# Optimization experiments

Hardware: AMD Instinct MI355X
Metric: run time of the kernel (lower is better)

The kernel has to match this reference:

```python
import jax, jax.numpy as jnp
import numpy as np

N_NODES = 50000
N_EDGES = 800000
NODE_DIM = 128
EDGE_DIM = 16
OUT_DIM = 64
HEADS = 4


def setup_inputs() -> dict:
    key = jax.random.key(0)
    ks = jax.random.split(key, 12)
    x = jax.random.normal(ks[0], (N_NODES, NODE_DIM), jnp.float32)
    edge_index = jax.random.randint(ks[1], (2, N_EDGES), 0, N_NODES)
    batch = jnp.zeros((N_NODES,), jnp.int32)
    edge_attr = jax.random.normal(ks[2], (N_EDGES, EDGE_DIM), jnp.float32)
    s = 1.0 / np.sqrt(NODE_DIM)
    W = jax.random.normal(ks[3], (NODE_DIM, HEADS * OUT_DIM), jnp.float32) * s
    att_src = jax.random.normal(ks[4], (HEADS, OUT_DIM), jnp.float32) * 0.1
    att_dst = jax.random.normal(ks[5], (HEADS, OUT_DIM), jnp.float32) * 0.1
    W_e = jax.random.normal(ks[6], (EDGE_DIM, HEADS * OUT_DIM), jnp.float32) * (1.0 / np.sqrt(EDGE_DIM))
    att_edge = jax.random.normal(ks[7], (HEADS, OUT_DIM), jnp.float32) * 0.1
    bias = jnp.zeros((OUT_DIM,), jnp.float32)
    gamma = jnp.ones((OUT_DIM,), jnp.float32)
    beta = jnp.zeros((OUT_DIM,), jnp.float32)
    return {"x": x, "edge_index": edge_index, "batch": batch, "edge_attr": edge_attr,
            "W": W, "att_src": att_src, "att_dst": att_dst, "W_e": W_e,
            "att_edge": att_edge, "bias": bias, "gamma": gamma, "beta": beta}


def reference(x, edge_index, batch, edge_attr, W, att_src, att_dst, W_e, att_edge, bias, gamma, beta):
    N = x.shape[0]
    H, C = att_src.shape
    src, dst = edge_index[0], edge_index[1]
    E = src.shape[0]

    # add self loops; self-loop edge_attr = per-node mean of incoming edge attrs (PyG fill_value='mean')
    cnt = jax.ops.segment_sum(jnp.ones((E, 1), x.dtype), dst, num_segments=N)
    loop_attr = jax.ops.segment_sum(edge_attr, dst, num_segments=N) / jnp.maximum(cnt, 1.0)
    loop_idx = jnp.arange(N, dtype=src.dtype)
    src_f = jnp.concatenate([src, loop_idx])
    dst_f = jnp.concatenate([dst, loop_idx])
    ea = jnp.concatenate([edge_attr, loop_attr], axis=0)

    h = (x @ W).reshape(N, H, C)                       # [N,H,C]
    a_src = jnp.einsum('nhc,hc->nh', h, att_src)       # [N,H]
    a_dst = jnp.einsum('nhc,hc->nh', h, att_dst)
    e_emb = (ea @ W_e).reshape(-1, H, C)               # [E',H,C]
    a_edge = jnp.einsum('ehc,hc->eh', e_emb, att_edge)

    alpha = jax.nn.leaky_relu(a_src[src_f] + a_dst[dst_f] + a_edge, 0.2)  # [E',H]
    amax = jax.ops.segment_max(alpha, dst_f, num_segments=N)
    expa = jnp.exp(alpha - amax[dst_f])
    denom = jax.ops.segment_sum(expa, dst_f, num_segments=N)
    att = expa / (denom[dst_f] + 1e-16)                # segment softmax over dst

    msg = h[src_f] * att[:, :, None]                   # [E',H,C]
    out = jax.ops.segment_sum(msg, dst_f, num_segments=N)  # [N,H,C]
    out = out.mean(axis=1) + bias                      # concat=False -> head mean

    mu = out.mean(-1, keepdims=True)
    var = out.var(-1, keepdims=True)
    out = (out - mu) / jnp.sqrt(var + 1e-5) * gamma + beta
    return jax.nn.elu(out)
```

## Files before the change

kernel.cpp:

```cpp
#include <hip/hip_runtime.h>

typedef unsigned int u32;
typedef unsigned short u16;

static constexpr int NN  = 50000;
static constexpr int EE  = 800000;
static constexpr int CAP = 64;

typedef __attribute__((ext_vector_type(8))) short bf16x8;
typedef __attribute__((ext_vector_type(4))) float f32x4;
typedef __attribute__((ext_vector_type(4))) u32   u32x4;

__device__ inline float u2f(u32 u){ union{u32 i; float f;} v; v.i=u; return v.f; }
__device__ inline float bf2f(u16 u){ return u2f(((u32)u)<<16); }
__device__ inline u16 f2bf(float f){ union{float f; u32 i;} v; v.f=f; u32 i=v.i;
    return (u16)((i + 0x7fffu + ((i>>16)&1u))>>16); }
__device__ inline u32 pk2(float a, float b){ return (u32)f2bf(a) | ((u32)f2bf(b)<<16); }
__device__ inline float lrelu(float x){ return x > 0.f ? x : 0.2f*x; }

__device__ inline u32 pkh(float a, float b){
    union{ _Float16 h[2]; u32 u; } v;
    v.h[0] = (_Float16)a; v.h[1] = (_Float16)b;
    return v.u;
}
__device__ inline float hlo(u32 u){ union{u32 u; _Float16 h[2];} v; v.u=u; return (float)v.h[0]; }
__device__ inline float hhi(u32 u){ union{u32 u; _Float16 h[2];} v; v.u=u; return (float)v.h[1]; }

__device__ inline float ld(const void* base, size_t i, int f32m){
    return f32m ? ((const float*)base)[i] : bf2f(((const u16*)base)[i]);
}

__device__ inline float wsum(float v){
    #pragma unroll
    for (int m=1;m<64;m<<=1) v += __shfl_xor(v, m, 64);
    return v;
}

#if defined(__has_builtin)
#if __has_builtin(__builtin_amdgcn_fdot2_f32_bf16)
#define HAS_DOT2 1
#endif
#endif

#ifdef HAS_DOT2
typedef __attribute__((ext_vector_type(2))) __bf16 bf16x2;
#endif

__device__ inline float dot2acc(u32 hv, u32 wv, float acc){
#ifdef HAS_DOT2
    union { u32 u; bf16x2 v; } a, b; a.u = hv; b.u = wv;
    return __builtin_amdgcn_fdot2_f32_bf16(a.v, b.v, acc, false);
#else
    acc = fmaf(u2f(hv<<16),         u2f(wv<<16),         acc);
    acc = fmaf(u2f(hv&0xffff0000u), u2f(wv&0xffff0000u), acc);
    return acc;
#endif
}

__device__ inline int detect_f32(const u16* xraw){
    int lane = threadIdx.x & 63;
    bool bad = false;
    #pragma unroll
    for (int i = 0; i < 8; ++i){
        float v = bf2f(xraw[2*(lane + i*64)]);
        if (!(fabsf(v) < 1e10f)) bad = true;
    }
    return __any(bad) ? 1 : 0;
}

__device__ inline void edge_logits(const void* ea, int e, int f32m,
                                   const float* __restrict__ Ml, float* A){
    float v[16];
    if (f32m){
        const f32x4* r = ((const f32x4*)ea) + (size_t)e*4;
        f32x4 a = __builtin_nontemporal_load(r);
        f32x4 b = __builtin_nontemporal_load(r+1);
        f32x4 c = __builtin_nontemporal_load(r+2);
        f32x4 d = __builtin_nontemporal_load(r+3);
        v[0]=a[0]; v[1]=a[1]; v[2]=a[2]; v[3]=a[3];
        v[4]=b[0]; v[5]=b[1]; v[6]=b[2]; v[7]=b[3];
        v[8]=c[0]; v[9]=c[1]; v[10]=c[2]; v[11]=c[3];
        v[12]=d[0]; v[13]=d[1]; v[14]=d[2]; v[15]=d[3];
    } else {
        const u32x4* r = ((const u32x4*)ea) + (size_t)e*2;
        u32x4 q0 = __builtin_nontemporal_load(r);
        u32x4 q1 = __builtin_nontemporal_load(r+1);
        v[0]=u2f(q0[0]<<16); v[1]=u2f(q0[0]&0xffff0000u);
        v[2]=u2f(q0[1]<<16); v[3]=u2f(q0[1]&0xffff0000u);
        v[4]=u2f(q0[2]<<16); v[5]=u2f(q0[2]&0xffff0000u);
        v[6]=u2f(q0[3]<<16); v[7]=u2f(q0[3]&0xffff0000u);
        v[8]=u2f(q1[0]<<16); v[9]=u2f(q1[0]&0xffff0000u);
        v[10]=u2f(q1[1]<<16); v[11]=u2f(q1[1]&0xffff0000u);
        v[12]=u2f(q1[2]<<16); v[13]=u2f(q1[2]&0xffff0000u);
        v[14]=u2f(q1[3]<<16); v[15]=u2f(q1[3]&0xffff0000u);
    }
    float a0=0,a1=0,a2=0,a3=0;
    #pragma unroll
    for (int j = 0; j < 16; ++j){
        a0 = fmaf(v[j], Ml[j*4+0], a0);
        a1 = fmaf(v[j], Ml[j*4+1], a1);
        a2 = fmaf(v[j], Ml[j*4+2], a2);
        a3 = fmaf(v[j], Ml[j*4+3], a3);
    }
    A[0]=a0; A[1]=a1; A[2]=a2; A[3]=a3;
}

__global__ __launch_bounds__(256) void k_prep(const u16* __restrict__ xraw,
                                              const void* __restrict__ W,
                                              const void* __restrict__ att_src,
                                              const void* __restrict__ att_dst,
                                              const void* __restrict__ W_e,
                                              const void* __restrict__ att_edge,
                                              int* __restrict__ flag,
                                              u16* __restrict__ Wt,
                                              float* __restrict__ Mv,
                                              int* __restrict__ deg){
    int f32m = detect_f32(xraw);
    int b = blockIdx.x, t = threadIdx.x;
    if (b == 0){
        if (t == 0) *flag = f32m;
        if (t < 64){
            int d = t >> 2, h = t & 3;
            float s = 0.f;
            for (int c = 0; c < 64; ++c)
                s += ld(W_e, d*256 + h*64 + c, f32m) * ld(att_edge, h*64 + c, f32m);
            Mv[t] = s;
        }
    } else if (b <= 128){
        int i = (b-1)*256 + t;
        int k = i >> 8, j = i & 255;
        int n = (j & 3)*64 + (j >> 2);
        Wt[j*128 + k] = f2bf(ld(W, (size_t)k*256 + n, f32m));
    } else if (b <= 136){
        int i = (b-129)*256 + t;
        int c = i >> 7, k = i & 127;
        float s = 0.f;
        if (c < 8){
            int h = c & 3;
            const void* att = (c < 4) ? att_src : att_dst;
            for (int j = 0; j < 64; ++j)
                s += ld(W, (size_t)k*256 + h*64 + j, f32m) * ld(att, h*64 + j, f32m);
        }
        Wt[(size_t)(256 + c)*128 + k] = f2bf(s);
    } else {
        int i = (b-137)*256 + t;
        if (i < NN) deg[i] = 0;
    }
}

__global__ __launch_bounds__(256) void k_gx(const void* __restrict__ x,
                                            const u16* __restrict__ Wt,
                                            const int* __restrict__ flag,
                                            u16* __restrict__ hbuf,
                                            float* __restrict__ a_src,
                                            float* __restrict__ a_dst,
                                            const int* __restrict__ ei,
                                            const void* __restrict__ ea,
                                            const float* __restrict__ Mv,
                                            int* __restrict__ deg,
                                            u32x4* __restrict__ erec,
                                            u32* __restrict__ bidx,
                                            int N, int E, int GB){
    int t = threadIdx.x;
    int f32m = *flag;
    int b = (int)blockIdx.x;
    bool isg; int wid;
    if (b < 2*GB){ isg = !(b & 1); wid = b >> 1; }
    else         { isg = false;    wid = b - GB; }
    if (isg){
        int row0 = wid*64;
        int wave = t >> 6, lane = t & 63;
        int l15 = lane & 15, quad = lane >> 4;
        int grow = row0 + wave*16 + l15; if (grow >= N) grow = N-1;
        bf16x8 afr[4];
        if (f32m){
            const f32x4* xf = (const f32x4*)x;
            #pragma unroll
            for (int s=0;s<4;++s){
                f32x4 v0 = __builtin_nontemporal_load(&xf[(size_t)grow*32 + s*8 + quad*2]);
                f32x4 v1 = __builtin_nontemporal_load(&xf[(size_t)grow*32 + s*8 + quad*2 + 1]);
                union{ u32x4 u; bf16x8 b; } cv;
                cv.u[0] = pk2(v0[0],v0[1]); cv.u[1] = pk2(v0[2],v0[3]);
                cv.u[2] = pk2(v1[0],v1[1]); cv.u[3] = pk2(v1[2],v1[3]);
                afr[s] = cv.b;
            }
        } else {
            const u16* x16 = (const u16*)x;
            #pragma unroll
            for (int s=0;s<4;++s)
                afr[s] = __builtin_nontemporal_load(
                    (const bf16x8*)&x16[(size_t)grow*128 + s*32 + quad*8]);
        }
        f32x4 acc[17];
        #pragma unroll
        for (int tl=0;tl<17;++tl){
            f32x4 a = {0.f,0.f,0.f,0.f};
            #pragma unroll
            for (int s=0;s<4;++s){
                bf16x8 bfr = *(const bf16x8*)&Wt[(size_t)(tl*16 + l15)*128 + s*32 + quad*8];
                a = __builtin_amdgcn_mfma_f32_16x16x32_bf16(afr[s], bfr, a, 0, 0, 0);
            }
            acc[tl] = a;
        }
        int rbase = row0 + wave*16 + quad*4;
        #pragma unroll
        for (int r=0;r<4;++r){
            int gr = rbase + r;
            if (gr < N){
                if (l15 < 4)
                    __builtin_nontemporal_store(acc[16][r], &a_src[gr*4 + l15]);
                else if (l15 < 8)
                    __builtin_nontemporal_store(acc[16][r], &a_dst[gr*4 + (l15-4)]);
            }
        }
        #pragma unroll
        for (int r=0;r<4;++r){
            int gr = rbase + r;
            if (gr < N){
                #pragma unroll
                for (int tl=0;tl<16;++tl)
                    __builtin_nontemporal_store(f2bf(acc[tl][r]),
                        &hbuf[(size_t)gr*256 + tl*16 + l15]);
            }
        }
    } else {
        int base = wid*512 + t;
        #pragma unroll
        for (int j=0;j<2;++j){
            int e = base + j*256;
            if (e >= E) continue;
            int src = __builtin_nontemporal_load(&ei[e]);
            int dst = __builtin_nontemporal_load(&ei[E + e]);
            int slot = atomicAdd(&deg[dst], 1);
            float A[4];
            edge_logits(ea, e, f32m, Mv, A);
            u32x4 rec;
            rec[0] = (u32)src; rec[1] = pkh(A[0],A[1]);
            rec[2] = pkh(A[2],A[3]); rec[3] = 0u;
            __builtin_nontemporal_store(rec, &erec[e]);
            if (slot < CAP)
                bidx[(size_t)dst*CAP + slot] = (u32)e;
        }
    }
}

__global__ __launch_bounds__(256) void k_node(const int* __restrict__ deg,
                                              const u32* __restrict__ bidx,
                                              const u32x4* __restrict__ erec,
                                              const float* __restrict__ a_src,
                                              const float* __restrict__ a_dst,
                                              const u16* __restrict__ hbuf,
                                              const void* __restrict__ bias,
                                              const void* __restrict__ gamma,
                                              const void* __restrict__ beta,
                                              const int* __restrict__ flag,
                                              void* __restrict__ out, int N){
    __shared__ uint4 lrec[4][CAP+4];
    int f32m = *flag;
    int lane = threadIdx.x & 63;
    int slot = threadIdx.x >> 6;
    int n = blockIdx.x*4 + slot;
    int dg = deg[n];
    int dc = dg < CAP ? dg : CAP;
    float4 an  = ((const float4*)a_src)[n];
    float4 adn = ((const float4*)a_dst)[n];
    bool v0 = lane < dc;
    u32 src = (u32)n;
    float w0=0.f,w1=0.f,w2=0.f,w3=0.f;
    float a0=0.f,a1=0.f,a2=0.f,a3=0.f;
    if (v0){
        u32 e = __builtin_nontemporal_load(&bidx[(size_t)n*CAP + lane]);
        u32x4 r = __builtin_nontemporal_load(&erec[e]);
        src = r[0];
        a0 = hlo(r[1]); a1 = hhi(r[1]); a2 = hlo(r[2]); a3 = hhi(r[2]);
        float4 asg = ((const float4*)a_src)[src];
        w0 = expf(lrelu(asg.x + adn.x + a0));
        w1 = expf(lrelu(asg.y + adn.y + a1));
        w2 = expf(lrelu(asg.z + adn.z + a2));
        w3 = expf(lrelu(asg.w + adn.w + a3));
    }
    float dn0 = wsum(w0), dn1 = wsum(w1), dn2 = wsum(w2), dn3 = wsum(w3);
    float invd = 1.f / (float)(dg > 1 ? dg : 1);
    float ge0 = wsum(a0)*invd, ge1 = wsum(a1)*invd;
    float ge2 = wsum(a2)*invd, ge3 = wsum(a3)*invd;
    float exS0 = expf(lrelu(an.x + adn.x + ge0));
    float exS1 = expf(lrelu(an.y + adn.y + ge1));
    float exS2 = expf(lrelu(an.z + adn.z + ge2));
    float exS3 = expf(lrelu(an.w + adn.w + ge3));
    float i0 = 0.25f/(dn0 + exS0 + 1e-16f);
    float i1 = 0.25f/(dn1 + exS1 + 1e-16f);
    float i2 = 0.25f/(dn2 + exS2 + 1e-16f);
    float i3 = 0.25f/(dn3 + exS3 + 1e-16f);
    if (v0)
        lrec[slot][lane] = make_uint4(src, pk2(w0*i0, w1*i1), pk2(w2*i2, w3*i3), 0u);
    if (lane == 0)
        lrec[slot][dc] = make_uint4((u32)n, pk2(exS0*i0, exS1*i1), pk2(exS2*i2, exS3*i3), 0u);
    else if (lane <= 3)
        lrec[slot][dc + lane] = make_uint4((u32)n, 0u, 0u, 0u);
    __syncthreads();
    int T = dc + 1;
    int iters = (T + 3) >> 2;
    int half = lane >> 5, l5 = lane & 31;
    const uint4* hb4 = (const uint4*)hbuf;
    float acc0 = 0.f, acc1 = 0.f;
    uint4 rA0 = lrec[slot][half];
    uint4 rA1 = lrec[slot][2 + half];
    uint4 hA0 = hb4[(size_t)rA0.x*32 + l5];
    uint4 hA1 = hb4[(size_t)rA1.x*32 + l5];
    uint4 rB0, rB1, hB0, hB1;
    if (iters > 1){
        rB0 = lrec[slot][4 + half];
        rB1 = lrec[slot][6 + half];
        hB0 = hb4[(size_t)rB0.x*32 + l5];
        hB1 = hb4[(size_t)rB1.x*32 + l5];
    }
    int i = 0;
    while (true){
        {
            bool pf = (i + 2 < iters);
            uint4 nr0, nr1, nh0, nh1;
            if (pf){
                nr0 = lrec[slot][4*(i+2) + half];
                nr1 = lrec[slot][4*(i+2) + 2 + half];
                nh0 = hb4[(size_t)nr0.x*32 + l5];
                nh1 = hb4[(size_t)nr1.x*32 + l5];
            }
            acc0 = dot2acc(hA0.x, rA0.y, acc0);
            acc0 = dot2acc(hA0.y, rA0.z, acc0);
            acc1 = dot2acc(hA0.z, rA0.y, acc1);
            acc1 = dot2acc(hA0.w, rA0.z, acc1);
            acc0 = dot2acc(hA1.x, rA1.y, acc0);
            acc0 = dot2acc(hA1.y, rA1.z, acc0);
            acc1 = dot2acc(hA1.z, rA1.y, acc1);
            acc1 = dot2acc(hA1.w, rA1.z, acc1);
            if (pf){ rA0=nr0; rA1=nr1; hA0=nh0; hA1=nh1; }
            if (++i >= iters) break;
        }
        {
            bool pf = (i + 2 < iters);
            uint4 nr0, nr1, nh0, nh1;
            if (pf){
                nr0 = lrec[slot][4*(i+2) + half];
                nr1 = lrec[slot][4*(i+2) + 2 + half];
                nh0 = hb4[(size_t)nr0.x*32 + l5];
                nh1 = hb4[(size_t)nr1.x*32 + l5];
            }
            acc0 = dot2acc(hB0.x, rB0.y, acc0);
            acc0 = dot2acc(hB0.y, rB0.z, acc0);
            acc1 = dot2acc(hB0.z, rB0.y, acc1);
            acc1 = dot2acc(hB0.w, rB0.z, acc1);
            acc0 = dot2acc(hB1.x, rB1.y, acc0);
            acc0 = dot2acc(hB1.y, rB1.z, acc0);
            acc1 = dot2acc(hB1.z, rB1.y, acc1);
            acc1 = dot2acc(hB1.w, rB1.z, acc1);
            if (pf){ rB0=nr0; rB1=nr1; hB0=nh0; hB1=nh1; }
            if (++i >= iters) break;
        }
    }
    acc0 += __shfl_xor(acc0, 32, 64);
    acc1 += __shfl_xor(acc1, 32, 64);
    float va = __shfl(acc0, lane>>1, 64);
    float vb = __shfl(acc1, lane>>1, 64);
    float o = ((lane & 1) ? vb : va) + ld(bias, lane, f32m);
    float mu = wsum(o) * (1.f/64.f);
    float d = o - mu;
    float var = wsum(d*d) * (1.f/64.f);
    float y = d * rsqrtf(var + 1e-5f) * ld(gamma, lane, f32m) + ld(beta, lane, f32m);
    y = y > 0.f ? y : expf(y) - 1.f;
    if (f32m) __builtin_nontemporal_store(y, &((float*)out)[(size_t)n*64 + lane]);
    else      __builtin_nontemporal_store(f2bf(y), &((u16*)out)[(size_t)n*64 + lane]);
}

extern "C" void kernel_launch(void* const* d_in, const int* in_sizes, int n_in,
                              void* d_out, int out_size, void* d_ws, size_t ws_size,
                              hipStream_t stream){
    const void* x        = d_in[0];
    const int*  ei       = (const int*)d_in[1];
    const void* ea       = d_in[3];
    const void* W        = d_in[4];
    const void* att_src  = d_in[5];
    const void* att_dst  = d_in[6];
    const void* W_e      = d_in[7];
    const void* att_edge = d_in[8];
    const void* bias     = d_in[9];
    const void* gamma    = d_in[10];
    const void* beta     = d_in[11];
    const int N = NN, E = EE;

    char* p = (char*)d_ws;
    auto alloc = [&](size_t bytes){ void* r = (void*)p; p += (bytes + 255) & ~(size_t)255; return r; };
    int*   deg   = (int*)  alloc((size_t)N*4);
    float* Mv    = (float*)alloc(64*4);
    float* a_src = (float*)alloc((size_t)N*16);
    float* a_dst = (float*)alloc((size_t)N*16);
    u32x4* erec  = (u32x4*)alloc((size_t)E*16);
    u32*   bidx  = (u32*)  alloc((size_t)N*CAP*4);
    u16*   hbuf  = (u16*)  alloc((size_t)N*256*2);
    u16*   Wt    = (u16*)  alloc((size_t)272*128*2);
    int*   flag  = (int*)  alloc(256);

    const int GB = (N + 63)/64;
    const int EB = (E + 511)/512;
    const int PB = 137 + (N + 255)/256;

    k_prep<<<PB, 256, 0, stream>>>((const u16*)x, W, att_src, att_dst, W_e, att_edge,
                                   flag, Wt, Mv, deg);
    k_gx<<<GB + EB, 256, 0, stream>>>(x, Wt, flag, hbuf, a_src, a_dst,
                                      ei, ea, Mv, deg, erec, bidx, N, E, GB);
    k_node<<<N/4, 256, 0, stream>>>(deg, bidx, erec, a_src, a_dst, hbuf,
                                    bias, gamma, beta, flag, d_out, N);
}
```

Before: 296.6 us.

## Two-pass bin the edges by destination range before CSR slot scatter

Edge records are no longer scattered straight into per-destination slots. Edges are first appended to coarse destination bins (512 nodes each, 8 replicated counter sets to cut contention), and a new k_bin kernel then scatters each bin's records into per-node slots, so deg atomics and writes hit a localized, cache-friendly region. The per-slot record now stores src and logits inline (12 bytes), which removes the indirect erec lookup in k_node. The cost is an extra kernel launch, an extra pass over about 12.8 MB of binned records, and an overflow fallback path.

```diff
diff --git a/kernel.cpp b/kernel.cpp
--- a/kernel.cpp
+++ b/kernel.cpp
@@ -6,6 +6,9 @@
 static constexpr int NN  = 50000;
 static constexpr int EE  = 800000;
 static constexpr int CAP = 64;
+static constexpr int NBIN = 128;
+static constexpr int NSET = 8;
+static constexpr int CAPB = 1536;
 
 typedef __attribute__((ext_vector_type(8))) short bf16x8;
 typedef __attribute__((ext_vector_type(4))) float f32x4;
@@ -114,7 +117,8 @@
                                               int* __restrict__ flag,
                                               u16* __restrict__ Wt,
                                               float* __restrict__ Mv,
-                                              int* __restrict__ deg){
+                                              int* __restrict__ deg,
+                                              u32* __restrict__ binCnt){
     int f32m = detect_f32(xraw);
     int b = blockIdx.x, t = threadIdx.x;
     if (b == 0){
@@ -145,6 +149,7 @@
     } else {
         int i = (b-137)*256 + t;
         if (i < NN) deg[i] = 0;
+        else if (i < NN + NSET*NBIN) binCnt[i - NN] = 0u;
     }
 }
 
@@ -158,8 +163,9 @@
                                             const void* __restrict__ ea,
                                             const float* __restrict__ Mv,
                                             int* __restrict__ deg,
-                                            u32x4* __restrict__ erec,
-                                            u32* __restrict__ bidx,
+                                            u32* __restrict__ binCnt,
+                                            u32x4* __restrict__ binBuf,
+                                            u32* __restrict__ brec3,
                                             int N, int E, int GB){
     int t = threadIdx.x;
     int f32m = *flag;
@@ -224,29 +230,54 @@
             }
         }
     } else {
-        int base = wid*512 + t;
-        #pragma unroll
-        for (int j=0;j<2;++j){
-            int e = base + j*256;
-            if (e >= E) continue;
+        int e = wid*256 + t;
+        if (e < E){
             int src = __builtin_nontemporal_load(&ei[e]);
             int dst = __builtin_nontemporal_load(&ei[E + e]);
-            int slot = atomicAdd(&deg[dst], 1);
+            int set = b & (NSET-1);
+            int bin = dst >> 9;
+            int pos = atomicAdd((int*)&binCnt[set*NBIN + bin], 1);
             float A[4];
             edge_logits(ea, e, f32m, Mv, A);
             u32x4 rec;
             rec[0] = (u32)src; rec[1] = pkh(A[0],A[1]);
-            rec[2] = pkh(A[2],A[3]); rec[3] = 0u;
-            __builtin_nontemporal_store(rec, &erec[e]);
-            if (slot < CAP)
-                bidx[(size_t)dst*CAP + slot] = (u32)e;
+            rec[2] = pkh(A[2],A[3]); rec[3] = (u32)dst;
+            if (pos < CAPB){
+                binBuf[(size_t)(set*NBIN + bin)*CAPB + pos] = rec;
+            } else {
+                int slot = atomicAdd(&deg[dst], 1);
+                if (slot < CAP){
+                    u32* bp = brec3 + ((size_t)dst*CAP + slot)*3;
+                    bp[0] = rec[0]; bp[1] = rec[1]; bp[2] = rec[2];
+                }
+            }
+        }
+    }
+}
+
+__global__ __launch_bounds__(1024) void k_bin(const u32* __restrict__ binCnt,
+                                              const u32x4* __restrict__ binBuf,
+                                              int* __restrict__ deg,
+                                              u32* __restrict__ brec3){
+    int bin = blockIdx.x;
+    int t = threadIdx.x;
+    for (int s = 0; s < NSET; ++s){
+        int cnt = (int)binCnt[s*NBIN + bin]; if (cnt > CAPB) cnt = CAPB;
+        const u32x4* buf = binBuf + (size_t)(s*NBIN + bin)*CAPB;
+        for (int i = t; i < cnt; i += 1024){
+            u32x4 r = buf[i];
+            int dst = (int)r[3];
+            int slot = atomicAdd(&deg[dst], 1);
+            if (slot < CAP){
+                u32* bp = brec3 + ((size_t)dst*CAP + slot)*3;
+                bp[0] = r[0]; bp[1] = r[1]; bp[2] = r[2];
+            }
         }
     }
 }
 
 __global__ __launch_bounds__(256) void k_node(const int* __restrict__ deg,
-                                              const u32* __restrict__ bidx,
-                                              const u32x4* __restrict__ erec,
+                                              const u32* __restrict__ brec3,
                                               const float* __restrict__ a_src,
                                               const float* __restrict__ a_dst,
                                               const u16* __restrict__ hbuf,
@@ -269,10 +300,12 @@
     float w0=0.f,w1=0.f,w2=0.f,w3=0.f;
     float a0=0.f,a1=0.f,a2=0.f,a3=0.f;
     if (v0){
-        u32 e = __builtin_nontemporal_load(&bidx[(size_t)n*CAP + lane]);
-        u32x4 r = __builtin_nontemporal_load(&erec[e]);
-        src = r[0];
-        a0 = hlo(r[1]); a1 = hhi(r[1]); a2 = hlo(r[2]); a3 = hhi(r[2]);
+        const u32* rp = brec3 + ((size_t)n*CAP + lane)*3;
+        u32 s   = __builtin_nontemporal_load(&rp[0]);
+        u32 p01 = __builtin_nontemporal_load(&rp[1]);
+        u32 p23 = __builtin_nontemporal_load(&rp[2]);
+        src = s;
+        a0 = hlo(p01); a1 = hhi(p01); a2 = hlo(p23); a3 = hhi(p23);
         float4 asg = ((const float4*)a_src)[src];
         w0 = expf(lrelu(asg.x + adn.x + a0));
         w1 = expf(lrelu(asg.y + adn.y + a1));
@@ -393,20 +426,23 @@
     float* Mv    = (float*)alloc(64*4);
     float* a_src = (float*)alloc((size_t)N*16);
     float* a_dst = (float*)alloc((size_t)N*16);
-    u32x4* erec  = (u32x4*)alloc((size_t)E*16);
-    u32*   bidx  = (u32*)  alloc((size_t)N*CAP*4);
+    u32*   brec3 = (u32*)  alloc((size_t)N*CAP*12);
+    u32x4* binBuf= (u32x4*)alloc((size_t)NSET*NBIN*CAPB*16);
+    u32*   binCnt= (u32*)  alloc((size_t)NSET*NBIN*4);
     u16*   hbuf  = (u16*)  alloc((size_t)N*256*2);
     u16*   Wt    = (u16*)  alloc((size_t)272*128*2);
     int*   flag  = (int*)  alloc(256);
 
     const int GB = (N + 63)/64;
-    const int EB = (E + 511)/512;
-    const int PB = 137 + (N + 255)/256;
+    const int EB = (E + 255)/256;
+    const int PB = 137 + (NN + NSET*NBIN + 255)/256;
 
     k_prep<<<PB, 256, 0, stream>>>((const u16*)x, W, att_src, att_dst, W_e, att_edge,
-                                   flag, Wt, Mv, deg);
+                                   flag, Wt, Mv, deg, binCnt);
     k_gx<<<GB + EB, 256, 0, stream>>>(x, Wt, flag, hbuf, a_src, a_dst,
-                                      ei, ea, Mv, deg, erec, bidx, N, E, GB);
-    k_node<<<N/4, 256, 0, stream>>>(deg, bidx, erec, a_src, a_dst, hbuf,
+                                      ei, ea, Mv, deg, binCnt, binBuf, brec3,
+                                      N, E, GB);
+    k_bin<<<NBIN, 1024, 0, stream>>>(binCnt, binBuf, deg, brec3);
+    k_node<<<N/4, 256, 0, stream>>>(deg, brec3, a_src, a_dst, hbuf,
                                     bias, gamma, beta, flag, d_out, N);
 }
```

Measured after the change: 431.4 us. 1.45x slower.

## Replace fixed-capacity bucket index with CSR built via count, scan, place

Applied to the files above, without the earlier changes.

Edge bucketing changes from a per-node fixed-capacity index array plus indirect record lookup to a compact CSR layout. Degrees are counted in k_gx into 8 striped counter sets to spread atomic contention, then prefix-summed by a two-kernel scan, and a placement kernel writes edge records contiguously by destination. k_node then reads records directly at start+lane, dropping the bidx indirection and the 64-slot-per-node buffer. This adds three kernel launches, a memset and a second pass over edge_index in exchange for coalesced, denser gathers in the node kernel.

```diff
diff --git a/kernel.cpp b/kernel.cpp
--- a/kernel.cpp
+++ b/kernel.cpp
@@ -6,6 +6,7 @@
 static constexpr int NN  = 50000;
 static constexpr int EE  = 800000;
 static constexpr int CAP = 64;
+static constexpr int NSET = 8;
 
 typedef __attribute__((ext_vector_type(8))) short bf16x8;
 typedef __attribute__((ext_vector_type(4))) float f32x4;
@@ -113,8 +114,7 @@
                                               const void* __restrict__ att_edge,
                                               int* __restrict__ flag,
                                               u16* __restrict__ Wt,
-                                              float* __restrict__ Mv,
-                                              int* __restrict__ deg){
+                                              float* __restrict__ Mv){
     int f32m = detect_f32(xraw);
     int b = blockIdx.x, t = threadIdx.x;
     if (b == 0){
@@ -131,7 +131,7 @@
         int k = i >> 8, j = i & 255;
         int n = (j & 3)*64 + (j >> 2);
         Wt[j*128 + k] = f2bf(ld(W, (size_t)k*256 + n, f32m));
-    } else if (b <= 136){
+    } else {
         int i = (b-129)*256 + t;
         int c = i >> 7, k = i & 127;
         float s = 0.f;
@@ -142,9 +142,6 @@
                 s += ld(W, (size_t)k*256 + h*64 + j, f32m) * ld(att, h*64 + j, f32m);
         }
         Wt[(size_t)(256 + c)*128 + k] = f2bf(s);
-    } else {
-        int i = (b-137)*256 + t;
-        if (i < NN) deg[i] = 0;
     }
 }
 
@@ -155,98 +152,163 @@
                                             float* __restrict__ a_src,
                                             float* __restrict__ a_dst,
                                             const int* __restrict__ ei,
-                                            const void* __restrict__ ea,
-                                            const float* __restrict__ Mv,
-                                            int* __restrict__ deg,
-                                            u32x4* __restrict__ erec,
-                                            u32* __restrict__ bidx,
-                                            int N, int E, int GB){
+                                            u32* __restrict__ deg8,
+                                            int N, int E, int EB){
     int t = threadIdx.x;
+    int b = (int)blockIdx.x;
+    if (b < EB){
+        int e = b*256 + t;
+        if (e < E){
+            int dst = __builtin_nontemporal_load(&ei[E + e]);
+            atomicAdd(&deg8[(size_t)(b & (NSET-1))*NN + dst], 1u);
+        }
+        return;
+    }
     int f32m = *flag;
-    int b = (int)blockIdx.x;
-    bool isg; int wid;
-    if (b < 2*GB){ isg = !(b & 1); wid = b >> 1; }
-    else         { isg = false;    wid = b - GB; }
-    if (isg){
-        int row0 = wid*64;
-        int wave = t >> 6, lane = t & 63;
-        int l15 = lane & 15, quad = lane >> 4;
-        int grow = row0 + wave*16 + l15; if (grow >= N) grow = N-1;
-        bf16x8 afr[4];
-        if (f32m){
-            const f32x4* xf = (const f32x4*)x;
+    int wid = b - EB;
+    int row0 = wid*64;
+    int wave = t >> 6, lane = t & 63;
+    int l15 = lane & 15, quad = lane >> 4;
+    int grow = row0 + wave*16 + l15; if (grow >= N) grow = N-1;
+    bf16x8 afr[4];
+    if (f32m){
+        const f32x4* xf = (const f32x4*)x;
+        #pragma unroll
+        for (int s=0;s<4;++s){
+            f32x4 v0 = __builtin_nontemporal_load(&xf[(size_t)grow*32 + s*8 + quad*2]);
+            f32x4 v1 = __builtin_nontemporal_load(&xf[(size_t)grow*32 + s*8 + quad*2 + 1]);
+            union{ u32x4 u; bf16x8 b; } cv;
+            cv.u[0] = pk2(v0[0],v0[1]); cv.u[1] = pk2(v0[2],v0[3]);
+            cv.u[2] = pk2(v1[0],v1[1]); cv.u[3] = pk2(v1[2],v1[3]);
+            afr[s] = cv.b;
+        }
+    } else {
+        const u16* x16 = (const u16*)x;
+        #pragma unroll
+        for (int s=0;s<4;++s)
+            afr[s] = __builtin_nontemporal_load(
+                (const bf16x8*)&x16[(size_t)grow*128 + s*32 + quad*8]);
+    }
+    f32x4 acc[17];
+    #pragma unroll
+    for (int tl=0;tl<17;++tl){
+        f32x4 a = {0.f,0.f,0.f,0.f};
+        #pragma unroll
+        for (int s=0;s<4;++s){
+            bf16x8 bfr = *(const bf16x8*)&Wt[(size_t)(tl*16 + l15)*128 + s*32 + quad*8];
+            a = __builtin_amdgcn_mfma_f32_16x16x32_bf16(afr[s], bfr, a, 0, 0, 0);
+        }
+        acc[tl] = a;
+    }
+    int rbase = row0 + wave*16 + quad*4;
+    #pragma unroll
+    for (int r=0;r<4;++r){
+        int gr = rbase + r;
+        if (gr < N){
+            if (l15 < 4)
+                __builtin_nontemporal_store(acc[16][r], &a_src[gr*4 + l15]);
+            else if (l15 < 8)
+                __builtin_nontemporal_store(acc[16][r], &a_dst[gr*4 + (l15-4)]);
+        }
+    }
+    #pragma unroll
+    for (int r=0;r<4;++r){
+        int gr = rbase + r;
+        if (gr < N){
             #pragma unroll
-            for (int s=0;s<4;++s){
-                f32x4 v0 = __builtin_nontemporal_load(&xf[(size_t)grow*32 + s*8 + quad*2]);
-                f32x4 v1 = __builtin_nontemporal_load(&xf[(size_t)grow*32 + s*8 + quad*2 + 1]);
-                union{ u32x4 u; bf16x8 b; } cv;
-                cv.u[0] = pk2(v0[0],v0[1]); cv.u[1] = pk2(v0[2],v0[3]);
-                cv.u[2] = pk2(v1[0],v1[1]); cv.u[3] = pk2(v1[2],v1[3]);
-                afr[s] = cv.b;
-            }
-        } else {
-            const u16* x16 = (const u16*)x;
-            #pragma unroll
-            for (int s=0;s<4;++s)
-                afr[s] = __builtin_nontemporal_load(
-                    (const bf16x8*)&x16[(size_t)grow*128 + s*32 + quad*8]);
-        }
-        f32x4 acc[17];
-        #pragma unroll
-        for (int tl=0;tl<17;++tl){
-            f32x4 a = {0.f,0.f,0.f,0.f};
-            #pragma unroll
-            for (int s=0;s<4;++s){
-                bf16x8 bfr = *(const bf16x8*)&Wt[(size_t)(tl*16 + l15)*128 + s*32 + quad*8];
-                a = __builtin_amdgcn_mfma_f32_16x16x32_bf16(afr[s], bfr, a, 0, 0, 0);
-            }
-            acc[tl] = a;
-        }
-        int rbase = row0 + wave*16 + quad*4;
-        #pragma unroll
-        for (int r=0;r<4;++r){
-            int gr = rbase + r;
-            if (gr < N){
-                if (l15 < 4)
-                    __builtin_nontemporal_store(acc[16][r], &a_src[gr*4 + l15]);
-                else if (l15 < 8)
-                    __builtin_nontemporal_store(acc[16][r], &a_dst[gr*4 + (l15-4)]);
-            }
-        }
-        #pragma unroll
-        for (int r=0;r<4;++r){
-            int gr = rbase + r;
-            if (gr < N){
-                #pragma unroll
-                for (int tl=0;tl<16;++tl)
-                    __builtin_nontemporal_store(f2bf(acc[tl][r]),
-                        &hbuf[(size_t)gr*256 + tl*16 + l15]);
-            }
-        }
-    } else {
-        int base = wid*512 + t;
-        #pragma unroll
-        for (int j=0;j<2;++j){
-            int e = base + j*256;
-            if (e >= E) continue;
-            int src = __builtin_nontemporal_load(&ei[e]);
-            int dst = __builtin_nontemporal_load(&ei[E + e]);
-            int slot = atomicAdd(&deg[dst], 1);
-            float A[4];
-            edge_logits(ea, e, f32m, Mv, A);
-            u32x4 rec;
-            rec[0] = (u32)src; rec[1] = pkh(A[0],A[1]);
-            rec[2] = pkh(A[2],A[3]); rec[3] = 0u;
-            __builtin_nontemporal_store(rec, &erec[e]);
-            if (slot < CAP)
-                bidx[(size_t)dst*CAP + slot] = (u32)e;
-        }
-    }
-}
-
-__global__ __launch_bounds__(256) void k_node(const int* __restrict__ deg,
-                                              const u32* __restrict__ bidx,
-                                              const u32x4* __restrict__ erec,
+            for (int tl=0;tl<16;++tl)
+                __builtin_nontemporal_store(f2bf(acc[tl][r]),
+                    &hbuf[(size_t)gr*256 + tl*16 + l15]);
+        }
+    }
+}
+
+__global__ __launch_bounds__(256) void k_scanA(const u32* __restrict__ deg8,
+                                               u32* __restrict__ bsum){
+    __shared__ u32 ws[4];
+    int b = blockIdx.x, t = threadIdx.x;
+    u32 s = 0;
+    int base = b*2048 + t*8;
+    #pragma unroll
+    for (int j=0;j<8;++j){
+        int i = base + j;
+        if (i < NSET*NN) s += deg8[(size_t)(i & 7)*NN + (i >> 3)];
+    }
+    #pragma unroll
+    for (int m=1;m<64;m<<=1) s += __shfl_xor(s, m, 64);
+    if ((t & 63) == 0) ws[t >> 6] = s;
+    __syncthreads();
+    if (t == 0) bsum[b] = ws[0] + ws[1] + ws[2] + ws[3];
+}
+
+__global__ __launch_bounds__(256) void k_scanB(const u32* __restrict__ deg8,
+                                               const u32* __restrict__ bsum,
+                                               u32* __restrict__ cur8,
+                                               u32* __restrict__ nstart){
+    __shared__ u32 ts[256];
+    __shared__ u32 ws[4];
+    int b = blockIdx.x, t = threadIdx.x;
+    u32 pb = (t < b) ? bsum[t] : 0u;
+    #pragma unroll
+    for (int m=1;m<64;m<<=1) pb += __shfl_xor(pb, m, 64);
+    if ((t & 63) == 0) ws[t >> 6] = pb;
+    __syncthreads();
+    u32 blockbase = ws[0] + ws[1] + ws[2] + ws[3];
+    u32 v[8]; u32 tsum = 0;
+    int base = b*2048 + t*8;
+    #pragma unroll
+    for (int j=0;j<8;++j){
+        int i = base + j;
+        v[j] = (i < NSET*NN) ? deg8[(size_t)(i & 7)*NN + (i >> 3)] : 0u;
+        tsum += v[j];
+    }
+    ts[t] = tsum;
+    __syncthreads();
+    for (int off=1; off<256; off<<=1){
+        u32 xv = (t >= off) ? ts[t-off] : 0u;
+        __syncthreads();
+        ts[t] += xv;
+        __syncthreads();
+    }
+    u32 run = blockbase + ts[t] - tsum;
+    #pragma unroll
+    for (int j=0;j<8;++j){
+        int i = base + j;
+        if (i < NSET*NN){
+            int n = i >> 3, s = i & 7;
+            cur8[(size_t)s*NN + n] = run;
+            if (s == 0) nstart[n] = run;
+            if (i == NSET*NN - 1) nstart[NN] = run + v[j];
+            run += v[j];
+        }
+    }
+}
+
+__global__ __launch_bounds__(256) void k_place(const int* __restrict__ ei,
+                                               const void* __restrict__ ea,
+                                               const float* __restrict__ Mv,
+                                               const int* __restrict__ flag,
+                                               u32* __restrict__ cur8,
+                                               u32x4* __restrict__ rec16,
+                                               int E){
+    int t = threadIdx.x;
+    int w = (int)blockIdx.x;
+    int e = w*256 + t;
+    if (e >= E) return;
+    int f32m = *flag;
+    int src = __builtin_nontemporal_load(&ei[e]);
+    int dst = __builtin_nontemporal_load(&ei[E + e]);
+    u32 pos = atomicAdd(&cur8[(size_t)(w & (NSET-1))*NN + dst], 1u);
+    float A[4];
+    edge_logits(ea, e, f32m, Mv, A);
+    u32x4 rec;
+    rec[0] = (u32)src; rec[1] = pkh(A[0],A[1]);
+    rec[2] = pkh(A[2],A[3]); rec[3] = 0u;
+    rec16[pos] = rec;
+}
+
+__global__ __launch_bounds__(256) void k_node(const u32* __restrict__ nstart,
+                                              const u32x4* __restrict__ rec16,
                                               const float* __restrict__ a_src,
                                               const float* __restrict__ a_dst,
                                               const u16* __restrict__ hbuf,
@@ -260,7 +322,8 @@
     int lane = threadIdx.x & 63;
     int slot = threadIdx.x >> 6;
     int n = blockIdx.x*4 + slot;
-    int dg = deg[n];
+    u32 start = nstart[n];
+    int dg = (int)(nstart[n+1] - start);
     int dc = dg < CAP ? dg : CAP;
     float4 an  = ((const float4*)a_src)[n];
     float4 adn = ((const float4*)a_dst)[n];
@@ -269,8 +332,7 @@
     float w0=0.f,w1=0.f,w2=0.f,w3=0.f;
     float a0=0.f,a1=0.f,a2=0.f,a3=0.f;
     if (v0){
-        u32 e = __builtin_nontemporal_load(&bidx[(size_t)n*CAP + lane]);
-        u32x4 r = __builtin_nontemporal_load(&erec[e]);
+        u32x4 r = rec16[start + lane];
         src = r[0];
         a0 = hlo(r[1]); a1 = hhi(r[1]); a2 = hlo(r[2]); a3 = hhi(r[2]);
         float4 asg = ((const float4*)a_src)[src];
@@ -389,24 +451,30 @@
 
     char* p = (char*)d_ws;
     auto alloc = [&](size_t bytes){ void* r = (void*)p; p += (bytes + 255) & ~(size_t)255; return r; };
-    int*   deg   = (int*)  alloc((size_t)N*4);
+    u32*   deg8  = (u32*)  alloc((size_t)NSET*N*4);
+    u32*   cur8  = (u32*)  alloc((size_t)NSET*N*4);
+    u32*   nstart= (u32*)  alloc((size_t)(N+1)*4);
+    u32*   bsum  = (u32*)  alloc((size_t)256*4);
     float* Mv    = (float*)alloc(64*4);
     float* a_src = (float*)alloc((size_t)N*16);
     float* a_dst = (float*)alloc((size_t)N*16);
-    u32x4* erec  = (u32x4*)alloc((size_t)E*16);
-    u32*   bidx  = (u32*)  alloc((size_t)N*CAP*4);
+    u32x4* rec16 = (u32x4*)alloc((size_t)E*16);
     u16*   hbuf  = (u16*)  alloc((size_t)N*256*2);
     u16*   Wt    = (u16*)  alloc((size_t)272*128*2);
     int*   flag  = (int*)  alloc(256);
 
+    const int EB = (E + 255)/256;
     const int GB = (N + 63)/64;
-    const int EB = (E + 511)/512;
-    const int PB = 137 + (N + 255)/256;
-
-    k_prep<<<PB, 256, 0, stream>>>((const u16*)x, W, att_src, att_dst, W_e, att_edge,
-                                   flag, Wt, Mv, deg);
-    k_gx<<<GB + EB, 256, 0, stream>>>(x, Wt, flag, hbuf, a_src, a_dst,
-                                      ei, ea, Mv, deg, erec, bidx, N, E, GB);
-    k_node<<<N/4, 256, 0, stream>>>(deg, bidx, erec, a_src, a_dst, hbuf,
+    const int SB = (NSET*N + 2047)/2048;
+
+    hipMemsetAsync(deg8, 0, (size_t)NSET*N*4, stream);
+    k_prep<<<137, 256, 0, stream>>>((const u16*)x, W, att_src, att_dst, W_e, att_edge,
+                                    flag, Wt, Mv);
+    k_gx<<<EB + GB, 256, 0, stream>>>(x, Wt, flag, hbuf, a_src, a_dst,
+                                      ei, deg8, N, E, EB);
+    k_scanA<<<SB, 256, 0, stream>>>(deg8, bsum);
+    k_scanB<<<SB, 256, 0, stream>>>(deg8, bsum, cur8, nstart);
+    k_place<<<EB, 256, 0, stream>>>(ei, ea, Mv, flag, cur8, rec16, E);
+    k_node<<<N/4, 256, 0, stream>>>(nstart, rec16, a_src, a_dst, hbuf,
                                     bias, gamma, beta, flag, d_out, N);
 }
```

Result: slower. 323.9 us (+9.2%).

## Fuse three phases into one cooperative persistent kernel with grid syncs

Applied to the files above, without the earlier changes.

Replaces the three separate launches (prep, gemm+edge scatter, node aggregation) with a single cooperative persistent kernel that loops over tiles and uses grid-wide syncs between phases, keeping a three-launch fallback. It also replaces the edge-record array plus per-node index list with direct per-node bucketed edge records, so the node phase makes one dependent load per edge instead of two. The aim is to remove launch gaps and an indirection. In exchange, the persistent loop limits occupancy to the co-resident grid, the grid syncs add cost, bucket writes become scattered, and the larger per-node record buffer uses more memory.

```diff
diff --git a/kernel.cpp b/kernel.cpp
--- a/kernel.cpp
+++ b/kernel.cpp
@@ -1,4 +1,7 @@
 #include <hip/hip_runtime.h>
+#include <hip/hip_cooperative_groups.h>
+
+namespace cg = cooperative_groups;
 
 typedef unsigned int u32;
 typedef unsigned short u16;
@@ -105,18 +108,16 @@
     A[0]=a0; A[1]=a1; A[2]=a2; A[3]=a3;
 }
 
-__global__ __launch_bounds__(256) void k_prep(const u16* __restrict__ xraw,
-                                              const void* __restrict__ W,
-                                              const void* __restrict__ att_src,
-                                              const void* __restrict__ att_dst,
-                                              const void* __restrict__ W_e,
-                                              const void* __restrict__ att_edge,
-                                              int* __restrict__ flag,
-                                              u16* __restrict__ Wt,
-                                              float* __restrict__ Mv,
-                                              int* __restrict__ deg){
+__device__ inline void prep_tile(int b, int t, const u16* xraw, const void* W,
+                                 const void* att_src, const void* att_dst,
+                                 const void* W_e, const void* att_edge,
+                                 int* flag, u16* Wt, float* Mv, int* deg, int N){
+    if (b >= 137){
+        int i = (b - 137)*256 + t;
+        if (i < N) deg[i] = 0;
+        return;
+    }
     int f32m = detect_f32(xraw);
-    int b = blockIdx.x, t = threadIdx.x;
     if (b == 0){
         if (t == 0) *flag = f32m;
         if (t < 64){
@@ -131,7 +132,7 @@
         int k = i >> 8, j = i & 255;
         int n = (j & 3)*64 + (j >> 2);
         Wt[j*128 + k] = f2bf(ld(W, (size_t)k*256 + n, f32m));
-    } else if (b <= 136){
+    } else {
         int i = (b-129)*256 + t;
         int c = i >> 7, k = i & 127;
         float s = 0.f;
@@ -142,124 +143,96 @@
                 s += ld(W, (size_t)k*256 + h*64 + j, f32m) * ld(att, h*64 + j, f32m);
         }
         Wt[(size_t)(256 + c)*128 + k] = f2bf(s);
+    }
+}
+
+__device__ inline void gemm_tile(int b, int t, int f32m, const void* x,
+                                 const u16* Wt, u16* hbuf,
+                                 float* a_src, float* a_dst, int N){
+    int row0 = b*64;
+    int wave = t >> 6, lane = t & 63;
+    int l15 = lane & 15, quad = lane >> 4;
+    int grow = row0 + wave*16 + l15; if (grow >= N) grow = N-1;
+    bf16x8 afr[4];
+    if (f32m){
+        const f32x4* xf = (const f32x4*)x;
+        #pragma unroll
+        for (int s=0;s<4;++s){
+            f32x4 v0 = __builtin_nontemporal_load(&xf[(size_t)grow*32 + s*8 + quad*2]);
+            f32x4 v1 = __builtin_nontemporal_load(&xf[(size_t)grow*32 + s*8 + quad*2 + 1]);
+            union{ u32x4 u; bf16x8 b; } cv;
+            cv.u[0] = pk2(v0[0],v0[1]); cv.u[1] = pk2(v0[2],v0[3]);
+            cv.u[2] = pk2(v1[0],v1[1]); cv.u[3] = pk2(v1[2],v1[3]);
+            afr[s] = cv.b;
+        }
     } else {
-        int i = (b-137)*256 + t;
-        if (i < NN) deg[i] = 0;
-    }
-}
-
-__global__ __launch_bounds__(256) void k_gx(const void* __restrict__ x,
-                                            const u16* __restrict__ Wt,
-                                            const int* __restrict__ flag,
-                                            u16* __restrict__ hbuf,
-                                            float* __restrict__ a_src,
-                                            float* __restrict__ a_dst,
-                                            const int* __restrict__ ei,
-                                            const void* __restrict__ ea,
-                                            const float* __restrict__ Mv,
-                                            int* __restrict__ deg,
-                                            u32x4* __restrict__ erec,
-                                            u32* __restrict__ bidx,
-                                            int N, int E, int GB){
-    int t = threadIdx.x;
-    int f32m = *flag;
-    int b = (int)blockIdx.x;
-    bool isg; int wid;
-    if (b < 2*GB){ isg = !(b & 1); wid = b >> 1; }
-    else         { isg = false;    wid = b - GB; }
-    if (isg){
-        int row0 = wid*64;
-        int wave = t >> 6, lane = t & 63;
-        int l15 = lane & 15, quad = lane >> 4;
-        int grow = row0 + wave*16 + l15; if (grow >= N) grow = N-1;
-        bf16x8 afr[4];
-        if (f32m){
-            const f32x4* xf = (const f32x4*)x;
+        const u16* x16 = (const u16*)x;
+        #pragma unroll
+        for (int s=0;s<4;++s)
+            afr[s] = __builtin_nontemporal_load(
+                (const bf16x8*)&x16[(size_t)grow*128 + s*32 + quad*8]);
+    }
+    f32x4 acc[17];
+    #pragma unroll
+    for (int tl=0;tl<17;++tl){
+        f32x4 a = {0.f,0.f,0.f,0.f};
+        #pragma unroll
+        for (int s=0;s<4;++s){
+            bf16x8 bfr = *(const bf16x8*)&Wt[(size_t)(tl*16 + l15)*128 + s*32 + quad*8];
+            a = __builtin_amdgcn_mfma_f32_16x16x32_bf16(afr[s], bfr, a, 0, 0, 0);
+        }
+        acc[tl] = a;
+    }
+    int rbase = row0 + wave*16 + quad*4;
+    #pragma unroll
+    for (int r=0;r<4;++r){
+        int gr = rbase + r;
+        if (gr < N){
+            if (l15 < 4)
+                __builtin_nontemporal_store(acc[16][r], &a_src[gr*4 + l15]);
+            else if (l15 < 8)
+                __builtin_nontemporal_store(acc[16][r], &a_dst[gr*4 + (l15-4)]);
+        }
+    }
+    #pragma unroll
+    for (int r=0;r<4;++r){
+        int gr = rbase + r;
+        if (gr < N){
             #pragma unroll
-            for (int s=0;s<4;++s){
-                f32x4 v0 = __builtin_nontemporal_load(&xf[(size_t)grow*32 + s*8 + quad*2]);
-                f32x4 v1 = __builtin_nontemporal_load(&xf[(size_t)grow*32 + s*8 + quad*2 + 1]);
-                union{ u32x4 u; bf16x8 b; } cv;
-                cv.u[0] = pk2(v0[0],v0[1]); cv.u[1] = pk2(v0[2],v0[3]);
-                cv.u[2] = pk2(v1[0],v1[1]); cv.u[3] = pk2(v1[2],v1[3]);
-                afr[s] = cv.b;
-            }
-        } else {
-            const u16* x16 = (const u16*)x;
-            #pragma unroll
-            for (int s=0;s<4;++s)
-                afr[s] = __builtin_nontemporal_load(
-                    (const bf16x8*)&x16[(size_t)grow*128 + s*32 + quad*8]);
-        }
-        f32x4 acc[17];
-        #pragma unroll
-        for (int tl=0;tl<17;++tl){
-            f32x4 a = {0.f,0.f,0.f,0.f};
-            #pragma unroll
-            for (int s=0;s<4;++s){
-                bf16x8 bfr = *(const bf16x8*)&Wt[(size_t)(tl*16 + l15)*128 + s*32 + quad*8];
-                a = __builtin_amdgcn_mfma_f32_16x16x32_bf16(afr[s], bfr, a, 0, 0, 0);
-            }
-            acc[tl] = a;
-        }
-        int rbase = row0 + wave*16 + quad*4;
-        #pragma unroll
-        for (int r=0;r<4;++r){
-            int gr = rbase + r;
-            if (gr < N){
-                if (l15 < 4)
-                    __builtin_nontemporal_store(acc[16][r], &a_src[gr*4 + l15]);
-                else if (l15 < 8)
-                    __builtin_nontemporal_store(acc[16][r], &a_dst[gr*4 + (l15-4)]);
-            }
-        }
-        #pragma unroll
-        for (int r=0;r<4;++r){
-            int gr = rbase + r;
-            if (gr < N){
-                #pragma unroll
-                for (int tl=0;tl<16;++tl)
-                    __builtin_nontemporal_store(f2bf(acc[tl][r]),
-                        &hbuf[(size_t)gr*256 + tl*16 + l15]);
-            }
-        }
-    } else {
-        int base = wid*512 + t;
-        #pragma unroll
-        for (int j=0;j<2;++j){
-            int e = base + j*256;
-            if (e >= E) continue;
-            int src = __builtin_nontemporal_load(&ei[e]);
-            int dst = __builtin_nontemporal_load(&ei[E + e]);
-            int slot = atomicAdd(&deg[dst], 1);
-            float A[4];
-            edge_logits(ea, e, f32m, Mv, A);
-            u32x4 rec;
-            rec[0] = (u32)src; rec[1] = pkh(A[0],A[1]);
-            rec[2] = pkh(A[2],A[3]); rec[3] = 0u;
-            __builtin_nontemporal_store(rec, &erec[e]);
-            if (slot < CAP)
-                bidx[(size_t)dst*CAP + slot] = (u32)e;
-        }
-    }
-}
-
-__global__ __launch_bounds__(256) void k_node(const int* __restrict__ deg,
-                                              const u32* __restrict__ bidx,
-                                              const u32x4* __restrict__ erec,
-                                              const float* __restrict__ a_src,
-                                              const float* __restrict__ a_dst,
-                                              const u16* __restrict__ hbuf,
-                                              const void* __restrict__ bias,
-                                              const void* __restrict__ gamma,
-                                              const void* __restrict__ beta,
-                                              const int* __restrict__ flag,
-                                              void* __restrict__ out, int N){
+            for (int tl=0;tl<16;++tl)
+                __builtin_nontemporal_store(f2bf(acc[tl][r]),
+                    &hbuf[(size_t)gr*256 + tl*16 + l15]);
+        }
+    }
+}
+
+__device__ inline void edge_tile(int w, int t, int f32m, const int* ei,
+                                 const void* ea, const float* Mv,
+                                 int* deg, u32x4* brec, int E){
+    int e = w*256 + t;
+    if (e >= E) return;
+    int src = __builtin_nontemporal_load(&ei[e]);
+    int dst = __builtin_nontemporal_load(&ei[E + e]);
+    int slot = atomicAdd(&deg[dst], 1);
+    float A[4];
+    edge_logits(ea, e, f32m, Mv, A);
+    if (slot < CAP){
+        u32x4 rec;
+        rec[0] = (u32)src; rec[1] = pkh(A[0],A[1]);
+        rec[2] = pkh(A[2],A[3]); rec[3] = 0u;
+        brec[(size_t)dst*CAP + slot] = rec;
+    }
+}
+
+__device__ inline void node_tile(int nb4, int t, int f32m, const int* deg,
+                                 const u32x4* brec, const float* a_src,
+                                 const float* a_dst, const u16* hbuf,
+                                 const void* bias, const void* gamma,
+                                 const void* beta, void* out, int N){
     __shared__ uint4 lrec[4][CAP+4];
-    int f32m = *flag;
-    int lane = threadIdx.x & 63;
-    int slot = threadIdx.x >> 6;
-    int n = blockIdx.x*4 + slot;
+    int lane = t & 63;
+    int slot = t >> 6;
+    int n = nb4*4 + slot;
     int dg = deg[n];
     int dc = dg < CAP ? dg : CAP;
     float4 an  = ((const float4*)a_src)[n];
@@ -269,8 +242,7 @@
     float w0=0.f,w1=0.f,w2=0.f,w3=0.f;
     float a0=0.f,a1=0.f,a2=0.f,a3=0.f;
     if (v0){
-        u32 e = __builtin_nontemporal_load(&bidx[(size_t)n*CAP + lane]);
-        u32x4 r = __builtin_nontemporal_load(&erec[e]);
+        u32x4 r = __builtin_nontemporal_load(&brec[(size_t)n*CAP + lane]);
         src = r[0];
         a0 = hlo(r[1]); a1 = hhi(r[1]); a2 = hlo(r[2]); a3 = hhi(r[2]);
         float4 asg = ((const float4*)a_src)[src];
@@ -371,6 +343,47 @@
     else      __builtin_nontemporal_store(f2bf(y), &((u16*)out)[(size_t)n*64 + lane]);
 }
 
+__global__ __launch_bounds__(256, 4) void k_all(const void* x, const int* ei,
+                                                const void* ea, const void* W,
+                                                const void* att_src, const void* att_dst,
+                                                const void* W_e, const void* att_edge,
+                                                const void* bias, const void* gamma,
+                                                const void* beta,
+                                                int* flag, u16* Wt, float* Mv,
+                                                int* deg, u32x4* brec,
+                                                float* a_src, float* a_dst,
+                                                u16* hbuf, void* out,
+                                                int N, int E, int phase){
+    int t = threadIdx.x;
+    int nb = gridDim.x;
+    const int ZB  = (N + 255)/256;
+    const int PT0 = 137 + ZB;
+    const int GB  = (N + 63)/64;
+    const int EB  = (E + 255)/256;
+    const int PT1 = GB + EB;
+    const int PT2 = N/4;
+    if (phase <= 0){
+        for (int b = blockIdx.x; b < PT0; b += nb)
+            prep_tile(b, t, (const u16*)x, W, att_src, att_dst, W_e, att_edge,
+                      flag, Wt, Mv, deg, N);
+    }
+    if (phase < 0){ __threadfence(); cg::this_grid().sync(); }
+    if (phase < 0 || phase == 1){
+        int f32m = *flag;
+        for (int b = blockIdx.x; b < PT1; b += nb){
+            if (b < GB) gemm_tile(b, t, f32m, x, Wt, hbuf, a_src, a_dst, N);
+            else        edge_tile(b - GB, t, f32m, ei, ea, Mv, deg, brec, E);
+        }
+    }
+    if (phase < 0){ __threadfence(); cg::this_grid().sync(); }
+    if (phase < 0 || phase == 2){
+        int f32m = *flag;
+        for (int b = blockIdx.x; b < PT2; b += nb)
+            node_tile(b, t, f32m, deg, brec, a_src, a_dst, hbuf,
+                      bias, gamma, beta, out, N);
+    }
+}
+
 extern "C" void kernel_launch(void* const* d_in, const int* in_sizes, int n_in,
                               void* d_out, int out_size, void* d_ws, size_t ws_size,
                               hipStream_t stream){
@@ -385,28 +398,54 @@
     const void* bias     = d_in[9];
     const void* gamma    = d_in[10];
     const void* beta     = d_in[11];
-    const int N = NN, E = EE;
 
     char* p = (char*)d_ws;
     auto alloc = [&](size_t bytes){ void* r = (void*)p; p += (bytes + 255) & ~(size_t)255; return r; };
-    int*   deg   = (int*)  alloc((size_t)N*4);
+    int*   deg   = (int*)  alloc((size_t)NN*4);
     float* Mv    = (float*)alloc(64*4);
-    float* a_src = (float*)alloc((size_t)N*16);
-    float* a_dst = (float*)alloc((size_t)N*16);
-    u32x4* erec  = (u32x4*)alloc((size_t)E*16);
-    u32*   bidx  = (u32*)  alloc((size_t)N*CAP*4);
-    u16*   hbuf  = (u16*)  alloc((size_t)N*256*2);
+    float* a_src = (float*)alloc((size_t)NN*16);
+    float* a_dst = (float*)alloc((size_t)NN*16);
+    u32x4* brec  = (u32x4*)alloc((size_t)NN*CAP*16);
+    u16*   hbuf  = (u16*)  alloc((size_t)NN*256*2);
     u16*   Wt    = (u16*)  alloc((size_t)272*128*2);
     int*   flag  = (int*)  alloc(256);
 
-    const int GB = (N + 63)/64;
-    const int EB = (E + 511)/512;
-    const int PB = 137 + (N + 255)/256;
-
-    k_prep<<<PB, 256, 0, stream>>>((const u16*)x, W, att_src, att_dst, W_e, att_edge,
-                                   flag, Wt, Mv, deg);
-    k_gx<<<GB + EB, 256, 0, stream>>>(x, Wt, flag, hbuf, a_src, a_dst,
-                                      ei, ea, Mv, deg, erec, bidx, N, E, GB);
-    k_node<<<N/4, 256, 0, stream>>>(deg, bidx, erec, a_src, a_dst, hbuf,
-                                    bias, gamma, beta, flag, d_out, N);
-}
+    int Nv = NN, Ev = EE;
+    const int PT0 = 137 + (NN + 255)/256;
+    const int PT1 = (NN + 63)/64 + (EE + 255)/256;
+    const int PT2 = NN/4;
+
+    int dev = 0; hipGetDevice(&dev);
+    int coop = 0; hipDeviceGetAttribute(&coop, hipDeviceAttributeCooperativeLaunch, dev);
+    int ncu = 256; hipDeviceGetAttribute(&ncu, hipDeviceAttributeMultiprocessorCount, dev);
+    int mb = 0;
+    hipOccupancyMaxActiveBlocksPerMultiprocessor(&mb, k_all, 256, 0);
+
+    bool done = false;
+    if (coop && mb > 0 && ncu > 0){
+        int grid = mb * ncu;
+        if (grid > PT2) grid = PT2;
+        int ph = -1;
+        void* args[] = { (void*)&x, (void*)&ei, (void*)&ea, (void*)&W,
+                         (void*)&att_src, (void*)&att_dst, (void*)&W_e,
+                         (void*)&att_edge, (void*)&bias, (void*)&gamma,
+                         (void*)&beta, (void*)&flag, (void*)&Wt, (void*)&Mv,
+                         (void*)&deg, (void*)&brec, (void*)&a_src, (void*)&a_dst,
+                         (void*)&hbuf, (void*)&d_out, (void*)&Nv, (void*)&Ev,
+                         (void*)&ph };
+        hipError_t e = hipLaunchCooperativeKernel((const void*)k_all, dim3(grid),
+                                                  dim3(256), args, 0, stream);
+        done = (e == hipSuccess);
+    }
+    if (!done){
+        k_all<<<PT0, 256, 0, stream>>>(x, ei, ea, W, att_src, att_dst, W_e, att_edge,
+                                       bias, gamma, beta, flag, Wt, Mv, deg, brec,
+                                       a_src, a_dst, hbuf, d_out, Nv, Ev, 0);
+        k_all<<<PT1, 256, 0, stream>>>(x, ei, ea, W, att_src, att_dst, W_e, att_edge,
+                                       bias, gamma, beta, flag, Wt, Mv, deg, brec,
+                                       a_src, a_dst, hbuf, d_out, Nv, Ev, 1);
+        k_all<<<PT2, 256, 0, stream>>>(x, ei, ea, W, att_src, att_dst, W_e, att_edge,
+                                       bias, gamma, beta, flag, Wt, Mv, deg, brec,
+                                       a_src, a_dst, hbuf, d_out, Nv, Ev, 2);
+    }
+}
```

Measured after the change: 606.5 us. +104.5%, slower.
